# Kernel optimization log

Hardware: AMD Instinct MI355X
Metric: run time of the kernel (lower is better)

## Reference

```python
import jax, jax.numpy as jnp
import numpy as np

NUM_HEADS = 8
LN_EPS = 1e-5


def setup_inputs() -> dict:
    key = jax.random.key(0)
    ks = jax.random.split(key, 9)
    B, C, H, W = 8, 512, 32, 32
    s = 1.0 / np.sqrt(C)
    return {
        "f_curr": jax.random.normal(ks[0], (B, C, H, W), dtype=jnp.float32),
        "f_prev": jax.random.normal(ks[1], (B, C, H, W), dtype=jnp.float32),
        "f_next": jax.random.normal(ks[2], (B, C, H, W), dtype=jnp.float32),
        "Wq": jax.random.normal(ks[3], (C, C), dtype=jnp.float32) * s,
        "Wk": jax.random.normal(ks[4], (C, C), dtype=jnp.float32) * s,
        "Wv": jax.random.normal(ks[5], (C, C), dtype=jnp.float32) * s,
        "Wo": jax.random.normal(ks[6], (C, C), dtype=jnp.float32) * s,
        "gamma": jnp.ones((C,), dtype=jnp.float32),
        "beta": jnp.zeros((C,), dtype=jnp.float32),
    }


def _flatten(f):
    # [B,C,H,W] -> [B, H*W, C]
    B, C, H, W = f.shape
    return f.reshape(B, C, H * W).transpose(0, 2, 1)


def reference(f_curr, f_prev, f_next, Wq, Wk, Wv, Wo, gamma, beta):
    B, C, H, W = f_curr.shape
    N = H * W
    hd = C // NUM_HEADS
    scale = hd ** -0.5

    curr_flat = _flatten(f_curr)                              # [B,N,C]
    neigh_flat = jnp.concatenate([_flatten(f_prev), _flatten(f_next)], axis=1)  # [B,2N,C]

    # torch Linear (no bias): y = x @ W.T
    Q = curr_flat @ Wq.T                                      # [B,N,C]
    K = neigh_flat @ Wk.T                                     # [B,2N,C]
    V = neigh_flat @ Wv.T                                     # [B,2N,C]

    def split_heads(t, L):
        return t.reshape(B, L, NUM_HEADS, hd).transpose(0, 2, 1, 3)  # [B,h,L,hd]

    Qh = split_heads(Q, N)
    Kh = split_heads(K, 2 * N)
    Vh = split_heads(V, 2 * N)

    scores = jnp.einsum("bhnd,bhmd->bhnm", Qh, Kh) * scale    # [B,h,N,2N]
    attn = jax.nn.softmax(scores, axis=-1)
    out = jnp.einsum("bhnm,bhmd->bhnd", attn, Vh)             # [B,h,N,hd]

    out = out.transpose(0, 2, 1, 3).reshape(B, N, C)          # merge heads
    out = curr_flat + out @ Wo.T                              # residual

    # LayerNorm over channel dim
    mu = jnp.mean(out, axis=-1, keepdims=True)
    var = jnp.mean(jnp.square(out - mu), axis=-1, keepdims=True)
    out = (out - mu) * jax.lax.rsqrt(var + LN_EPS) * gamma + beta

    return out.transpose(0, 2, 1).reshape(B, C, H, W)
```

## Files before the change

### kernel.cpp

```cpp
#include <hip/hip_runtime.h>
#include <hip/hip_bf16.h>
#include <math.h>

#define NH 8
#define HD 64
#define CH 512
#define NT 1024
#define NB 8

typedef __bf16 bf16_t;
typedef bf16_t bf16x8 __attribute__((ext_vector_type(8)));
typedef bf16_t bf16x4 __attribute__((ext_vector_type(4)));
typedef float  f32x4  __attribute__((ext_vector_type(4)));
typedef float  f32x16 __attribute__((ext_vector_type(16)));
typedef unsigned u32x4 __attribute__((ext_vector_type(4)));

#define MFMA16(a, b, c) __builtin_amdgcn_mfma_f32_16x16x32_bf16((a), (b), (c), 0, 0, 0)
#define MFMA32(a, b, c) __builtin_amdgcn_mfma_f32_32x32x16_bf16((a), (b), (c), 0, 0, 0)
#define EXP2(x) __builtin_amdgcn_exp2f(x)

__device__ __forceinline__ void gload16(const void* g, void* l) {
    __builtin_amdgcn_global_load_lds(
        (const __attribute__((address_space(1))) void*)g,
        (__attribute__((address_space(3))) void*)l, 16, 0, 0);
}

__device__ __forceinline__ unsigned cvtpk(float lo, float hi) {
    unsigned r;
    asm("v_cvt_pk_bf16_f32 %0, %1, %2" : "=v"(r) : "v"(lo), "v"(hi));
    return r;
}

__device__ __forceinline__ void plswap(unsigned& a, unsigned& b) {
    asm("v_permlane32_swap_b32 %0, %1" : "+v"(a), "+v"(b));
}

__global__ __launch_bounds__(256) void prep_kernel(
    const float* __restrict__ fc, const float* __restrict__ fp,
    const float* __restrict__ fn, bf16_t* __restrict__ Xc,
    bf16_t* __restrict__ Xn)
{
    __shared__ __align__(16) bf16_t tile[64 * 64];
    const int t = threadIdx.x;
    const int y = blockIdx.y;
    const int b = y / 3, ft = y % 3;
    const int c0 = (blockIdx.x & 7) * 64;
    const int n0 = (blockIdx.x >> 3) * 64;

    const float* src; bf16_t* dst;
    if (ft == 0)      { src = fc + (size_t)b * CH * NT; dst = Xc + (size_t)b * NT * CH; }
    else if (ft == 1) { src = fp + (size_t)b * CH * NT; dst = Xn + (size_t)b * 2 * NT * CH; }
    else              { src = fn + (size_t)b * CH * NT; dst = Xn + (size_t)b * 2 * NT * CH + (size_t)NT * CH; }

    const int nb = t & 15, cb = t >> 4;
    float4 ld[4];
#pragma unroll
    for (int i = 0; i < 4; ++i)
        ld[i] = *(const float4*)(src + (size_t)(c0 + cb * 4 + i) * NT + n0 + nb * 4);
    const float* lf = (const float*)ld;
#pragma unroll
    for (int j = 0; j < 4; ++j) {
        int n = nb * 4 + j;
        int v = (n >> 2) & 14;
        bf16x4 wv = { (bf16_t)lf[0 * 4 + j], (bf16_t)lf[1 * 4 + j],
                      (bf16_t)lf[2 * 4 + j], (bf16_t)lf[3 * 4 + j] };
        *(bf16x4*)(tile + n * 64 + ((cb ^ v) * 4)) = wv;
    }
    __syncthreads();
#pragma unroll
    for (int i = 0; i < 2; ++i) {
        int gid = t + i * 256;
        int n = gid >> 3, c16 = gid & 7;
        int v = (n >> 2) & 14;
        bf16x8 val = *(const bf16x8*)(tile + n * 64 + (((2 * c16) ^ v) * 4));
        *(bf16x8*)(dst + (size_t)(n0 + n) * CH + c0 + c16 * 8) = val;
    }
}

__global__ __launch_bounds__(256) void wcvt_kernel(
    const float* __restrict__ Wq, const float* __restrict__ Wk,
    const float* __restrict__ Wv, const float* __restrict__ Wo,
    bf16_t* __restrict__ Wb, float* __restrict__ SQz)
{
    const int m = blockIdx.y;
    const float* src = (m == 0) ? Wq : (m == 1) ? Wk : (m == 2) ? Wv : Wo;
    bf16_t* dst = Wb + (size_t)m * CH * CH;
    int gid = blockIdx.x * 256 + threadIdx.x;
    float4 v = *(const float4*)(src + (size_t)gid * 4);
    bf16x4 o = { (bf16_t)v.x, (bf16_t)v.y, (bf16_t)v.z, (bf16_t)v.w };
    *(bf16x4*)(dst + (size_t)gid * 4) = o;
    if (m == 0 && blockIdx.x < 16) {
        f32x4 zz = {0.f, 0.f, 0.f, 0.f};
        *(f32x4*)(SQz + (size_t)(blockIdx.x * 256 + threadIdx.x) * 4) = zz;
    }
}

template <bool SWAP>
__device__ __forceinline__ void gemm_core(const bf16_t* __restrict__ A,
                                          const bf16_t* __restrict__ B,
                                          bf16_t* aT0, bf16_t* bT0,
                                          bf16_t* aT1, bf16_t* bT1,
                                          f32x4 acc[4][4])
{
    const int t = threadIdx.x, w = t >> 6, lane = t & 63;
    const int lid = lane & 15, quad = lane >> 4;
    const int wm = w >> 1, wn = w & 1;
    const int l4 = lane >> 2, k4 = lane & 3;

#define GSTAGE(k0, aT, bT)                                                     \
    {                                                                          \
        _Pragma("unroll")                                                      \
        for (int i = 0; i < 2; ++i) {                                          \
            int q = w * 2 + i;                                 \
            int row = q * 16 + l4;                                             \
            int kk = k4 ^ ((row >> 1) & 3);                                    \
            gload16(A + (size_t)row * CH + (k0) + kk * 8, (aT) + q * 512);     \
            gload16(B + (size_t)row * CH + (k0) + kk * 8, (bT) + q * 512);     \
        }                                                                      \
    }

    GSTAGE(0, aT0, bT0);
    __syncthreads();

    for (int kt = 0; kt < 16; ++kt) {
        const int cur = kt & 1;
        const bf16_t* aTr = cur ? aT1 : aT0;
        const bf16_t* bTr = cur ? bT1 : bT0;
        if (kt < 15) {
            bf16_t* aTw = cur ? aT0 : aT1;
            bf16_t* bTw = cur ? bT0 : bT1;
            GSTAGE((kt + 1) * 32, aTw, bTw);
        }

        const bf16_t* mT = SWAP ? bTr : aTr;
        const bf16_t* nT = SWAP ? aTr : bTr;
        bf16x8 mf[4], nf[4];
#pragma unroll
        for (int i = 0; i < 4; ++i) {
            int row = wm * 64 + i * 16 + lid;
            int kw = quad ^ ((row >> 1) & 3);
            mf[i] = *(const bf16x8*)(mT + row * 32 + kw * 8);
        }
#pragma unroll
        for (int i = 0; i < 4; ++i) {
            int row = wn * 64 + i * 16 + lid;
            int kw = quad ^ ((row >> 1) & 3);
            nf[i] = *(const bf16x8*)(nT + row * 32 + kw * 8);
        }
        __builtin_amdgcn_s_setprio(1);
#pragma unroll
        for (int mi = 0; mi < 4; ++mi)
#pragma unroll
            for (int ni = 0; ni < 4; ++ni)
                acc[mi][ni] = MFMA16(mf[mi], nf[ni], acc[mi][ni]);
        __builtin_amdgcn_s_setprio(0);
        __syncthreads();
    }
#undef GSTAGE
}

__global__ __launch_bounds__(256) void qkv_kernel(
    const bf16_t* __restrict__ Xc, const bf16_t* __restrict__ Xn,
    const bf16_t* __restrict__ Wb,
    bf16_t* __restrict__ Qn, bf16_t* __restrict__ Kn, bf16_t* __restrict__ Vt)
{
    __shared__ __align__(16) bf16_t aT0[128 * 32];
    __shared__ __align__(16) bf16_t bT0[128 * 32];
    __shared__ __align__(16) bf16_t aT1[128 * 32];
    __shared__ __align__(16) bf16_t bT1[128 * 32];
    const int bx = blockIdx.x, b = blockIdx.y;
    const int t = threadIdx.x, w = t >> 6, lane = t & 63;
    const int lid = lane & 15, quad = lane >> 4;
    const int wm = w >> 1, wn = w & 1;
    const float QSC = 0.125f * 1.44269504f;

    f32x4 acc[4][4] = {};

    if (bx < 96) {
        const bf16_t* A; const bf16_t* B; bf16_t* O; float scale;
        if (bx < 32) {
            int nt = bx >> 2, ct = bx & 3;
            A = Xc + (size_t)b * NT * CH + (size_t)nt * 128 * CH;
            B = Wb + (size_t)0 * CH * CH + (size_t)ct * 128 * CH;
            O = Qn + (size_t)b * NT * CH + (size_t)nt * 128 * CH + ct * 128;
            scale = QSC;
        } else {
            int j = bx - 32, nt = j >> 2, ct = j & 3;
            A = Xn + (size_t)b * 2 * NT * CH + (size_t)nt * 128 * CH;
            B = Wb + (size_t)1 * CH * CH + (size_t)ct * 128 * CH;
            O = Kn + (size_t)b * 2 * NT * CH + (size_t)nt * 128 * CH + ct * 128;
            scale = 1.0f;
        }
        gemm_core<false>(A, B, aT0, bT0, aT1, bT1, acc);
#pragma unroll
        for (int mi = 0; mi < 4; ++mi)
#pragma unroll
            for (int ni = 0; ni < 4; ++ni)
#pragma unroll
                for (int r = 0; r < 4; ++r) {
                    int n  = wm * 64 + mi * 16 + quad * 4 + r;
                    int co = wn * 64 + ni * 16 + lid;
                    O[(size_t)n * CH + co] = (bf16_t)(acc[mi][ni][r] * scale);
                }
    } else {
        int j = bx - 96, nt = j >> 2, ct = j & 3;
        const bf16_t* A = Xn + (size_t)b * 2 * NT * CH + (size_t)nt * 128 * CH;
        const bf16_t* B = Wb + (size_t)2 * CH * CH + (size_t)ct * 128 * CH;
        bf16_t* O = Vt + (size_t)b * CH * 2 * NT + (size_t)ct * 128 * 2 * NT + nt * 128;
        gemm_core<true>(A, B, aT0, bT0, aT1, bT1, acc);
#pragma unroll
        for (int mi = 0; mi < 4; ++mi)
#pragma unroll
            for (int ni = 0; ni < 4; ++ni)
#pragma unroll
                for (int r = 0; r < 4; ++r) {
                    int co_l  = wm * 64 + mi * 16 + quad * 4 + r;
                    int key_l = wn * 64 + ni * 16 + lid;
                    O[(size_t)co_l * (2 * NT) + key_l] = (bf16_t)acc[mi][ni][r];
                }
    }
}

__global__ __launch_bounds__(256, 2) void attn_kernel(
    const bf16_t* __restrict__ Qn, const bf16_t* __restrict__ Kn,
    const bf16_t* __restrict__ Vt, bf16_t* __restrict__ AOn)
{
    __shared__ __align__(16) char smem[65536];
    bf16_t* const kbuf0 = (bf16_t*)smem;
    bf16_t* const kbuf1 = (bf16_t*)(smem + 16384);
    bf16_t* const vbuf0 = (bf16_t*)(smem + 32768);
    bf16_t* const vbuf1 = (bf16_t*)(smem + 49152);
    float*  const scr_all = (float*)smem;
    bf16_t* const obuf    = (bf16_t*)(smem + 36864);
    float*  const l_scr   = (float*)(smem + 55296);

    const int t = threadIdx.x;
    const int w = t >> 6, lane = t & 63;
    const int wq = w >> 1, wk = w & 1;
    const int l31 = lane & 31, h = lane >> 5;

    const int bid = blockIdx.x;
    const int xcd = bid & 7, ii = bid >> 3;
    const int grp = xcd * 8 + (ii >> 3);
    const int qt  = ii & 7;
    const int b = grp >> 3, hh = grp & 7;
    const int q0 = qt * 128;

    const bf16_t* Qb  = Qn + ((size_t)b * NT + q0) * CH + hh * HD;
    const bf16_t* Kb  = Kn + (size_t)b * 2 * NT * CH + hh * HD;
    const bf16_t* Vtb = Vt + ((size_t)b * CH + hh * HD) * (2 * NT);
    bf16_t* AOb = AOn + ((size_t)b * NT + q0) * CH + hh * HD;

#define STAGE_KV(kbn, kw, vw)                                                  \
    {                                                                          \
        _Pragma("unroll")                                                      \
        for (int i = 0; i < 4; ++i) {                                          \
            int ck = w * 64 + i * 256 + lane;                                  \
            int kr = ck >> 3, kg = ck & 7;                                     \
            gload16(Kb + (size_t)((kbn) + kr) * CH + ((kg ^ (kr & 7)) * 8),    \
                    (kw) + (w * 64 + i * 256) * 8);                            \
            int cv = ck;                                                       \
            int vr = cv >> 4, vg = cv & 15;                                    \
            gload16(Vtb + (size_t)vr * (2 * NT) + (kbn) + ((vg ^ (vr & 15)) * 8), \
                    (vw) + (w * 64 + i * 256) * 8);                            \
        }                                                                      \
    }

    const bf16_t* Qrow = Qb + (size_t)(wq * 64 + l31) * CH + h * 8;
    bf16x8 qf[2][4];
#pragma unroll
    for (int nf = 0; nf < 2; ++nf)
#pragma unroll
        for (int ks = 0; ks < 4; ++ks)
            qf[nf][ks] = *(const bf16x8*)(Qrow + (size_t)nf * 32 * CH + ks * 16);

    STAGE_KV(0, kbuf0, vbuf0);
    __syncthreads();

    f32x16 o[2][2] = {};
    float lpart[2] = {0.f, 0.f};

    const int swk = l31 & 7;
    const int swv = l31 & 15;

    for (int kt = 0; kt < 16; ++kt) {
        const int cur = kt & 1;
        const bf16_t* const kr_buf = cur ? kbuf1 : kbuf0;
        const bf16_t* const vr_buf = cur ? vbuf1 : vbuf0;
        bf16_t* const kw_buf = cur ? kbuf0 : kbuf1;
        bf16_t* const vw_buf = cur ? vbuf0 : vbuf1;

        if (kt < 15)
            STAGE_KV((kt + 1) * 128, kw_buf, vw_buf);

#pragma unroll
        for (int mf = 0; mf < 2; ++mf) {
            const int krow = wk * 64 + mf * 32 + l31;
            bf16x8 kfm[4];
#pragma unroll
            for (int ks = 0; ks < 4; ++ks)
                kfm[ks] = *(const bf16x8*)(kr_buf + krow * 64 + (((ks * 2 + h) ^ swk) * 8));

            f32x16 s[2] = {};
            __builtin_amdgcn_s_setprio(1);
#pragma unroll
            for (int ks = 0; ks < 4; ++ks)
#pragma unroll
                for (int nf = 0; nf < 2; ++nf)
                    s[nf] = MFMA32(kfm[ks], qf[nf][ks], s[nf]);
            __builtin_amdgcn_s_setprio(0);

            bf16x8 pfrag[2][2];
#pragma unroll
            for (int nf = 0; nf < 2; ++nf) {
                float p[16];
#pragma unroll
                for (int r = 0; r < 16; ++r) p[r] = EXP2(s[nf][r]);
                lpart[nf] += ((p[0] + p[1]) + (p[2] + p[3]))
                           + ((p[4] + p[5]) + (p[6] + p[7]))
                           + ((p[8] + p[9]) + (p[10] + p[11]))
                           + ((p[12] + p[13]) + (p[14] + p[15]));
                unsigned a0 = cvtpk(p[0], p[1]),   b0 = cvtpk(p[4], p[5]);
                unsigned a1 = cvtpk(p[2], p[3]),   b1 = cvtpk(p[6], p[7]);
                unsigned a2 = cvtpk(p[8], p[9]),   b2 = cvtpk(p[12], p[13]);
                unsigned a3 = cvtpk(p[10], p[11]), b3 = cvtpk(p[14], p[15]);
                plswap(a0, b0); plswap(a1, b1); plswap(a2, b2); plswap(a3, b3);
                u32x4 f0 = { a0, a1, b0, b1 };
                u32x4 f1 = { a2, a3, b2, b3 };
                pfrag[nf][0] = __builtin_bit_cast(bf16x8, f0);
                pfrag[nf][1] = __builtin_bit_cast(bf16x8, f1);
            }

            __builtin_amdgcn_s_setprio(1);
#pragma unroll
            for (int fi = 0; fi < 2; ++fi) {
                const int ks = mf * 2 + fi;
                bf16x8 av[2];
#pragma unroll
                for (int df = 0; df < 2; ++df) {
                    int vrow = df * 32 + l31;
                    av[df] = *(const bf16x8*)(vr_buf + vrow * 128 +
                             (((wk * 8 + ks * 2 + h) ^ swv) * 8));
                }
#pragma unroll
                for (int df = 0; df < 2; ++df)
#pragma unroll
                    for (int nf = 0; nf < 2; ++nf)
                        o[df][nf] = MFMA32(av[df], pfrag[nf][fi], o[df][nf]);
            }
            __builtin_amdgcn_s_setprio(0);
        }
        __syncthreads();
    }
#undef STAGE_KV

    float l2[2];
#pragma unroll
    for (int nf = 0; nf < 2; ++nf)
        l2[nf] = lpart[nf] + __shfl_xor(lpart[nf], 32);

    if (wk == 1) {
        float* scr = scr_all + wq * 4352;
#pragma unroll
        for (int df = 0; df < 2; ++df)
#pragma unroll
            for (int nf = 0; nf < 2; ++nf) {
                int qrow = nf * 32 + l31;
#pragma unroll
                for (int g = 0; g < 4; ++g) {
                    int d = df * 32 + 8 * g + 4 * h;
                    f32x4 v = { o[df][nf][4 * g + 0], o[df][nf][4 * g + 1],
                                o[df][nf][4 * g + 2], o[df][nf][4 * g + 3] };
                    *(f32x4*)(scr + qrow * 68 + d) = v;
                }
            }
        if (h == 0) {
            l_scr[wq * 64 + 0 * 32 + l31] = l2[0];
            l_scr[wq * 64 + 1 * 32 + l31] = l2[1];
        }
    }
    __syncthreads();

    if (wk == 0) {
        const float* scr = scr_all + wq * 4352;
        float inv[2];
#pragma unroll
        for (int nf = 0; nf < 2; ++nf)
            inv[nf] = 1.0f / (l2[nf] + l_scr[wq * 64 + nf * 32 + l31]);
#pragma unroll
        for (int df = 0; df < 2; ++df)
#pragma unroll
            for (int nf = 0; nf < 2; ++nf) {
                int qrow = nf * 32 + l31;
#pragma unroll
                for (int g = 0; g < 4; ++g) {
                    int d = df * 32 + 8 * g + 4 * h;
                    f32x4 part = *(const f32x4*)(scr + qrow * 68 + d);
                    bf16x4 ov = {
                        (bf16_t)((o[df][nf][4 * g + 0] + part.x) * inv[nf]),
                        (bf16_t)((o[df][nf][4 * g + 1] + part.y) * inv[nf]),
                        (bf16_t)((o[df][nf][4 * g + 2] + part.z) * inv[nf]),
                        (bf16_t)((o[df][nf][4 * g + 3] + part.w) * inv[nf]) };
                    int qg = wq * 64 + qrow;
                    *(bf16x4*)(obuf + qg * 72 + (d ^ (qg & 24))) = ov;
                }
            }
    }
    __syncthreads();

#pragma unroll
    for (int i = 0; i < 4; ++i) {
        int gid = t + i * 256;
        int qr = gid >> 3, c8 = (gid & 7) * 8;
        *(bf16x8*)(AOb + (size_t)qr * CH + c8) =
            *(const bf16x8*)(obuf + qr * 72 + (c8 ^ (qr & 24)));
    }
}

__global__ __launch_bounds__(256) void proj_kernel(
    const bf16_t* __restrict__ AOn, const bf16_t* __restrict__ Wb,
    const float* __restrict__ fc, float* __restrict__ Zt,
    float* __restrict__ Ssum, float* __restrict__ Ssq)
{
    __shared__ __align__(16) bf16_t aT0[128 * 32];
    __shared__ __align__(16) bf16_t bT0[128 * 32];
    __shared__ __align__(16) bf16_t aT1[128 * 32];
    __shared__ __align__(16) bf16_t bT1[128 * 32];
    const int bx = blockIdx.x, b = blockIdx.y;
    const int nt = bx >> 2, ct = bx & 3;
    const int t = threadIdx.x, w = t >> 6, lane = t & 63;
    const int lid = lane & 15, quad = lane >> 4;
    const int wm = w >> 1, wn = w & 1;

    const bf16_t* A = AOn + (size_t)b * NT * CH + (size_t)nt * 128 * CH;
    const bf16_t* B = Wb + (size_t)3 * CH * CH + (size_t)ct * 128 * CH;

    f32x4 acc[4][4] = {};
    gemm_core<true>(A, B, aT0, bT0, aT1, bT1, acc);

    const size_t bofs = (size_t)b * CH * NT;
    float sP[4] = {0.f, 0.f, 0.f, 0.f}, qP[4] = {0.f, 0.f, 0.f, 0.f};
#pragma unroll
    for (int mi = 0; mi < 4; ++mi)
#pragma unroll
        for (int ni = 0; ni < 4; ++ni)
#pragma unroll
            for (int r = 0; r < 4; ++r) {
                int co_l = wm * 64 + mi * 16 + quad * 4 + r;
                int n_l  = wn * 64 + ni * 16 + lid;
                size_t idx = bofs + (size_t)(ct * 128 + co_l) * NT + nt * 128 + n_l;
                float z = acc[mi][ni][r] + fc[idx];
                Zt[idx] = z;
                sP[ni] += z;
                qP[ni] += z * z;
            }
#pragma unroll
    for (int ni = 0; ni < 4; ++ni) {
        sP[ni] += __shfl_xor(sP[ni], 16);  sP[ni] += __shfl_xor(sP[ni], 32);
        qP[ni] += __shfl_xor(qP[ni], 16);  qP[ni] += __shfl_xor(qP[ni], 32);
    }
    __syncthreads();
    float* sRed = (float*)aT0;
    float* qRed = sRed + 256;
    if (quad == 0) {
#pragma unroll
        for (int ni = 0; ni < 4; ++ni) {
            sRed[w * 64 + ni * 16 + lid] = sP[ni];
            qRed[w * 64 + ni * 16 + lid] = qP[ni];
        }
    }
    __syncthreads();
    if (t < 128) {
        float s = sRed[t] + sRed[128 + t];
        float q = qRed[t] + qRed[128 + t];
        atomicAdd(&Ssum[(size_t)b * NT + nt * 128 + t], s);
        atomicAdd(&Ssq [(size_t)b * NT + nt * 128 + t], q);
    }
}

__global__ __launch_bounds__(256) void apply_kernel(
    const float* __restrict__ Zt, const float* __restrict__ Ssum,
    const float* __restrict__ Ssq, const float* __restrict__ gamma,
    const float* __restrict__ beta, float* __restrict__ out)
{
    const int row = blockIdx.x;
    const int co = row & 511, b = row >> 9;
    const int t = threadIdx.x;
    const float g = gamma[co], be = beta[co];
    const size_t base = (size_t)row * NT + t * 4;
    f32x4 z  = *(const f32x4*)(Zt + base);
    f32x4 S  = *(const f32x4*)(Ssum + (size_t)b * NT + t * 4);
    f32x4 Q2 = *(const f32x4*)(Ssq  + (size_t)b * NT + t * 4);
    f32x4 o;
#pragma unroll
    for (int c = 0; c < 4; ++c) {
        float mu  = S[c] * (1.0f / 512.0f);
        float var = Q2[c] * (1.0f / 512.0f) - mu * mu;
        float rs  = rsqrtf(var + 1e-5f);
        o[c] = (z[c] - mu) * rs * g + be;
    }
    *(f32x4*)(out + base) = o;
}

extern "C" void kernel_launch(void* const* d_in, const int* in_sizes, int n_in,
                              void* d_out, int out_size, void* d_ws, size_t ws_size,
                              hipStream_t stream)
{
    (void)in_sizes; (void)n_in; (void)out_size; (void)ws_size;
    const float* fc    = (const float*)d_in[0];
    const float* fp    = (const float*)d_in[1];
    const float* fn    = (const float*)d_in[2];
    const float* Wq    = (const float*)d_in[3];
    const float* Wk    = (const float*)d_in[4];
    const float* Wv    = (const float*)d_in[5];
    const float* Wo    = (const float*)d_in[6];
    const float* gamma = (const float*)d_in[7];
    const float* beta  = (const float*)d_in[8];
    float* out = (float*)d_out;

    char* ws = (char*)d_ws;
    bf16_t* Xn  = (bf16_t*)(ws);
    bf16_t* Qn  = (bf16_t*)(ws + 16777216);
    bf16_t* Kn  = (bf16_t*)(ws + 25165824);
    bf16_t* Xc  = (bf16_t*)(ws + 41943040);
    bf16_t* AOn = Xc;
    bf16_t* Vt  = (bf16_t*)(ws + 50331648);
    bf16_t* Wb  = (bf16_t*)(ws + 67108864);
    float*  Ssum = (float*)(ws + 69206016);
    float*  Ssq  = (float*)(ws + 69238784);
    float*  Zt  = (float*)(ws);

    prep_kernel<<<dim3(128, 24), 256, 0, stream>>>(fc, fp, fn, Xc, Xn);
    wcvt_kernel<<<dim3(256, 4), 256, 0, stream>>>(Wq, Wk, Wv, Wo, Wb, Ssum);
    qkv_kernel<<<dim3(160, 8), 256, 0, stream>>>(Xc, Xn, Wb, Qn, Kn, Vt);
    attn_kernel<<<dim3(512), 256, 0, stream>>>(Qn, Kn, Vt, AOn);
    proj_kernel<<<dim3(32, 8), 256, 0, stream>>>(AOn, Wb, fc, Zt, Ssum, Ssq);
    apply_kernel<<<4096, 256, 0, stream>>>(Zt, Ssum, Ssq, gamma, beta, out);
}
```

Before: 207.5 us.

## Halve attention tile sizes to double block count and occupancy

The attention kernel moves from 128-query by 128-key tiles to 64-query by 64-key tiles, halving shared memory to 32KB and raising launch bounds to 4 blocks per CU, with 1024 blocks instead of 512. The aim is more resident waves and better latency hiding on the many-CU GPU. In exchange, each K/V tile is reused by half as many queries, so K/V traffic from L2 doubles, there are twice as many loop iterations and barriers, and the V swizzle layout is changed to match.

```diff
diff --git a/kernel.cpp b/kernel.cpp
--- a/kernel.cpp
+++ b/kernel.cpp
@@ -221,18 +221,18 @@
     }
 }
 
-__global__ __launch_bounds__(256, 2) void attn_kernel(
+__global__ __launch_bounds__(256, 4) void attn_kernel(
     const bf16_t* __restrict__ Qn, const bf16_t* __restrict__ Kn,
     const bf16_t* __restrict__ Vt, bf16_t* __restrict__ AOn)
 {
-    __shared__ __align__(16) char smem[65536];
+    __shared__ __align__(16) char smem[32768];
     bf16_t* const kbuf0 = (bf16_t*)smem;
-    bf16_t* const kbuf1 = (bf16_t*)(smem + 16384);
-    bf16_t* const vbuf0 = (bf16_t*)(smem + 32768);
-    bf16_t* const vbuf1 = (bf16_t*)(smem + 49152);
+    bf16_t* const kbuf1 = (bf16_t*)(smem + 8192);
+    bf16_t* const vbuf0 = (bf16_t*)(smem + 16384);
+    bf16_t* const vbuf1 = (bf16_t*)(smem + 24576);
     float*  const scr_all = (float*)smem;
-    bf16_t* const obuf    = (bf16_t*)(smem + 36864);
-    float*  const l_scr   = (float*)(smem + 55296);
+    bf16_t* const obuf    = (bf16_t*)(smem + 17920);
+    float*  const l_scr   = (float*)(smem + 27136);
 
     const int t = threadIdx.x;
     const int w = t >> 6, lane = t & 63;
@@ -241,10 +241,10 @@
 
     const int bid = blockIdx.x;
     const int xcd = bid & 7, ii = bid >> 3;
-    const int grp = xcd * 8 + (ii >> 3);
-    const int qt  = ii & 7;
+    const int grp = xcd * 8 + (ii >> 4);
+    const int qt  = ii & 15;
     const int b = grp >> 3, hh = grp & 7;
-    const int q0 = qt * 128;
+    const int q0 = qt * 64;
 
     const bf16_t* Qb  = Qn + ((size_t)b * NT + q0) * CH + hh * HD;
     const bf16_t* Kb  = Kn + (size_t)b * 2 * NT * CH + hh * HD;
@@ -254,162 +254,127 @@
 #define STAGE_KV(kbn, kw, vw)                                                  \
     {                                                                          \
         _Pragma("unroll")                                                      \
-        for (int i = 0; i < 4; ++i) {                                          \
+        for (int i = 0; i < 2; ++i) {                                          \
             int ck = w * 64 + i * 256 + lane;                                  \
             int kr = ck >> 3, kg = ck & 7;                                     \
             gload16(Kb + (size_t)((kbn) + kr) * CH + ((kg ^ (kr & 7)) * 8),    \
                     (kw) + (w * 64 + i * 256) * 8);                            \
-            int cv = ck;                                                       \
-            int vr = cv >> 4, vg = cv & 15;                                    \
-            gload16(Vtb + (size_t)vr * (2 * NT) + (kbn) + ((vg ^ (vr & 15)) * 8), \
+            gload16(Vtb + (size_t)kr * (2 * NT) + (kbn) + ((kg ^ (kr & 7)) * 8), \
                     (vw) + (w * 64 + i * 256) * 8);                            \
         }                                                                      \
     }
 
-    const bf16_t* Qrow = Qb + (size_t)(wq * 64 + l31) * CH + h * 8;
-    bf16x8 qf[2][4];
-#pragma unroll
-    for (int nf = 0; nf < 2; ++nf)
-#pragma unroll
-        for (int ks = 0; ks < 4; ++ks)
-            qf[nf][ks] = *(const bf16x8*)(Qrow + (size_t)nf * 32 * CH + ks * 16);
+    const bf16_t* Qrow = Qb + (size_t)(wq * 32 + l31) * CH + h * 8;
+    bf16x8 qf[4];
+#pragma unroll
+    for (int ks = 0; ks < 4; ++ks)
+        qf[ks] = *(const bf16x8*)(Qrow + ks * 16);
 
     STAGE_KV(0, kbuf0, vbuf0);
     __syncthreads();
 
-    f32x16 o[2][2] = {};
-    float lpart[2] = {0.f, 0.f};
-
-    const int swk = l31 & 7;
-    const int swv = l31 & 15;
-
-    for (int kt = 0; kt < 16; ++kt) {
+    f32x16 o[2] = {};
+    float lpart = 0.f;
+
+    for (int kt = 0; kt < 32; ++kt) {
         const int cur = kt & 1;
         const bf16_t* const kr_buf = cur ? kbuf1 : kbuf0;
         const bf16_t* const vr_buf = cur ? vbuf1 : vbuf0;
         bf16_t* const kw_buf = cur ? kbuf0 : kbuf1;
         bf16_t* const vw_buf = cur ? vbuf0 : vbuf1;
 
-        if (kt < 15)
-            STAGE_KV((kt + 1) * 128, kw_buf, vw_buf);
-
-#pragma unroll
-        for (int mf = 0; mf < 2; ++mf) {
-            const int krow = wk * 64 + mf * 32 + l31;
-            bf16x8 kfm[4];
-#pragma unroll
-            for (int ks = 0; ks < 4; ++ks)
-                kfm[ks] = *(const bf16x8*)(kr_buf + krow * 64 + (((ks * 2 + h) ^ swk) * 8));
-
-            f32x16 s[2] = {};
-            __builtin_amdgcn_s_setprio(1);
-#pragma unroll
-            for (int ks = 0; ks < 4; ++ks)
-#pragma unroll
-                for (int nf = 0; nf < 2; ++nf)
-                    s[nf] = MFMA32(kfm[ks], qf[nf][ks], s[nf]);
-            __builtin_amdgcn_s_setprio(0);
-
-            bf16x8 pfrag[2][2];
-#pragma unroll
-            for (int nf = 0; nf < 2; ++nf) {
-                float p[16];
-#pragma unroll
-                for (int r = 0; r < 16; ++r) p[r] = EXP2(s[nf][r]);
-                lpart[nf] += ((p[0] + p[1]) + (p[2] + p[3]))
-                           + ((p[4] + p[5]) + (p[6] + p[7]))
-                           + ((p[8] + p[9]) + (p[10] + p[11]))
-                           + ((p[12] + p[13]) + (p[14] + p[15]));
-                unsigned a0 = cvtpk(p[0], p[1]),   b0 = cvtpk(p[4], p[5]);
-                unsigned a1 = cvtpk(p[2], p[3]),   b1 = cvtpk(p[6], p[7]);
-                unsigned a2 = cvtpk(p[8], p[9]),   b2 = cvtpk(p[12], p[13]);
-                unsigned a3 = cvtpk(p[10], p[11]), b3 = cvtpk(p[14], p[15]);
-                plswap(a0, b0); plswap(a1, b1); plswap(a2, b2); plswap(a3, b3);
-                u32x4 f0 = { a0, a1, b0, b1 };
-                u32x4 f1 = { a2, a3, b2, b3 };
-                pfrag[nf][0] = __builtin_bit_cast(bf16x8, f0);
-                pfrag[nf][1] = __builtin_bit_cast(bf16x8, f1);
+        if (kt < 31)
+            STAGE_KV((kt + 1) * 64, kw_buf, vw_buf);
+
+        const int krow = wk * 32 + l31;
+        bf16x8 kfm[4];
+#pragma unroll
+        for (int ks = 0; ks < 4; ++ks)
+            kfm[ks] = *(const bf16x8*)(kr_buf + krow * 64 + (((ks * 2 + h) ^ (krow & 7)) * 8));
+
+        f32x16 s = {};
+        __builtin_amdgcn_s_setprio(1);
+#pragma unroll
+        for (int ks = 0; ks < 4; ++ks)
+            s = MFMA32(kfm[ks], qf[ks], s);
+        __builtin_amdgcn_s_setprio(0);
+
+        float p[16];
+#pragma unroll
+        for (int r = 0; r < 16; ++r) p[r] = EXP2(s[r]);
+        lpart += ((p[0] + p[1]) + (p[2] + p[3]))
+               + ((p[4] + p[5]) + (p[6] + p[7]))
+               + ((p[8] + p[9]) + (p[10] + p[11]))
+               + ((p[12] + p[13]) + (p[14] + p[15]));
+        unsigned a0 = cvtpk(p[0], p[1]),   b0 = cvtpk(p[4], p[5]);
+        unsigned a1 = cvtpk(p[2], p[3]),   b1 = cvtpk(p[6], p[7]);
+        unsigned a2 = cvtpk(p[8], p[9]),   b2 = cvtpk(p[12], p[13]);
+        unsigned a3 = cvtpk(p[10], p[11]), b3 = cvtpk(p[14], p[15]);
+        plswap(a0, b0); plswap(a1, b1); plswap(a2, b2); plswap(a3, b3);
+        u32x4 f0 = { a0, a1, b0, b1 };
+        u32x4 f1 = { a2, a3, b2, b3 };
+        bf16x8 pfrag0 = __builtin_bit_cast(bf16x8, f0);
+        bf16x8 pfrag1 = __builtin_bit_cast(bf16x8, f1);
+
+        __builtin_amdgcn_s_setprio(1);
+#pragma unroll
+        for (int fi = 0; fi < 2; ++fi) {
+            const bf16x8 pf = fi ? pfrag1 : pfrag0;
+            bf16x8 av[2];
+#pragma unroll
+            for (int df = 0; df < 2; ++df) {
+                int vrow = df * 32 + l31;
+                int g = wk * 4 + fi * 2 + h;
+                av[df] = *(const bf16x8*)(vr_buf + vrow * 64 + ((g ^ (vrow & 7)) * 8));
             }
-
-            __builtin_amdgcn_s_setprio(1);
-#pragma unroll
-            for (int fi = 0; fi < 2; ++fi) {
-                const int ks = mf * 2 + fi;
-                bf16x8 av[2];
-#pragma unroll
-                for (int df = 0; df < 2; ++df) {
-                    int vrow = df * 32 + l31;
-                    av[df] = *(const bf16x8*)(vr_buf + vrow * 128 +
-                             (((wk * 8 + ks * 2 + h) ^ swv) * 8));
-                }
-#pragma unroll
-                for (int df = 0; df < 2; ++df)
-#pragma unroll
-                    for (int nf = 0; nf < 2; ++nf)
-                        o[df][nf] = MFMA32(av[df], pfrag[nf][fi], o[df][nf]);
+#pragma unroll
+            for (int df = 0; df < 2; ++df)
+                o[df] = MFMA32(av[df], pf, o[df]);
+        }
+        __builtin_amdgcn_s_setprio(0);
+        __syncthreads();
+    }
+#undef STAGE_KV
+
+    float l2 = lpart + __shfl_xor(lpart, 32);
+
+    if (wk == 1) {
+        float* scr = scr_all + wq * 2176;
+#pragma unroll
+        for (int df = 0; df < 2; ++df)
+#pragma unroll
+            for (int g = 0; g < 4; ++g) {
+                int d = df * 32 + 8 * g + 4 * h;
+                f32x4 v = { o[df][4 * g + 0], o[df][4 * g + 1],
+                            o[df][4 * g + 2], o[df][4 * g + 3] };
+                *(f32x4*)(scr + l31 * 68 + d) = v;
             }
-            __builtin_amdgcn_s_setprio(0);
-        }
-        __syncthreads();
-    }
-#undef STAGE_KV
-
-    float l2[2];
-#pragma unroll
-    for (int nf = 0; nf < 2; ++nf)
-        l2[nf] = lpart[nf] + __shfl_xor(lpart[nf], 32);
-
-    if (wk == 1) {
-        float* scr = scr_all + wq * 4352;
+        if (h == 0) l_scr[wq * 32 + l31] = l2;
+    }
+    __syncthreads();
+
+    if (wk == 0) {
+        const float* scr = scr_all + wq * 2176;
+        float inv = 1.0f / (l2 + l_scr[wq * 32 + l31]);
 #pragma unroll
         for (int df = 0; df < 2; ++df)
 #pragma unroll
-            for (int nf = 0; nf < 2; ++nf) {
-                int qrow = nf * 32 + l31;
-#pragma unroll
-                for (int g = 0; g < 4; ++g) {
-                    int d = df * 32 + 8 * g + 4 * h;
-                    f32x4 v = { o[df][nf][4 * g + 0], o[df][nf][4 * g + 1],
-                                o[df][nf][4 * g + 2], o[df][nf][4 * g + 3] };
-                    *(f32x4*)(scr + qrow * 68 + d) = v;
-                }
+            for (int g = 0; g < 4; ++g) {
+                int d = df * 32 + 8 * g + 4 * h;
+                f32x4 part = *(const f32x4*)(scr + l31 * 68 + d);
+                bf16x4 ov = {
+                    (bf16_t)((o[df][4 * g + 0] + part.x) * inv),
+                    (bf16_t)((o[df][4 * g + 1] + part.y) * inv),
+                    (bf16_t)((o[df][4 * g + 2] + part.z) * inv),
+                    (bf16_t)((o[df][4 * g + 3] + part.w) * inv) };
+                int qg = wq * 32 + l31;
+                *(bf16x4*)(obuf + qg * 72 + (d ^ (qg & 24))) = ov;
             }
-        if (h == 0) {
-            l_scr[wq * 64 + 0 * 32 + l31] = l2[0];
-            l_scr[wq * 64 + 1 * 32 + l31] = l2[1];
-        }
-    }
-    __syncthreads();
-
-    if (wk == 0) {
-        const float* scr = scr_all + wq * 4352;
-        float inv[2];
-#pragma unroll
-        for (int nf = 0; nf < 2; ++nf)
-            inv[nf] = 1.0f / (l2[nf] + l_scr[wq * 64 + nf * 32 + l31]);
-#pragma unroll
-        for (int df = 0; df < 2; ++df)
-#pragma unroll
-            for (int nf = 0; nf < 2; ++nf) {
-                int qrow = nf * 32 + l31;
-#pragma unroll
-                for (int g = 0; g < 4; ++g) {
-                    int d = df * 32 + 8 * g + 4 * h;
-                    f32x4 part = *(const f32x4*)(scr + qrow * 68 + d);
-                    bf16x4 ov = {
-                        (bf16_t)((o[df][nf][4 * g + 0] + part.x) * inv[nf]),
-                        (bf16_t)((o[df][nf][4 * g + 1] + part.y) * inv[nf]),
-                        (bf16_t)((o[df][nf][4 * g + 2] + part.z) * inv[nf]),
-                        (bf16_t)((o[df][nf][4 * g + 3] + part.w) * inv[nf]) };
-                    int qg = wq * 64 + qrow;
-                    *(bf16x4*)(obuf + qg * 72 + (d ^ (qg & 24))) = ov;
-                }
-            }
-    }
-    __syncthreads();
-
-#pragma unroll
-    for (int i = 0; i < 4; ++i) {
+    }
+    __syncthreads();
+
+#pragma unroll
+    for (int i = 0; i < 2; ++i) {
         int gid = t + i * 256;
         int qr = gid >> 3, c8 = (gid & 7) * 8;
         *(bf16x8*)(AOb + (size_t)qr * CH + c8) =
@@ -533,7 +498,7 @@
     prep_kernel<<<dim3(128, 24), 256, 0, stream>>>(fc, fp, fn, Xc, Xn);
     wcvt_kernel<<<dim3(256, 4), 256, 0, stream>>>(Wq, Wk, Wv, Wo, Wb, Ssum);
     qkv_kernel<<<dim3(160, 8), 256, 0, stream>>>(Xc, Xn, Wb, Qn, Kn, Vt);
-    attn_kernel<<<dim3(512), 256, 0, stream>>>(Qn, Kn, Vt, AOn);
+    attn_kernel<<<dim3(1024), 256, 0, stream>>>(Qn, Kn, Vt, AOn);
     proj_kernel<<<dim3(32, 8), 256, 0, stream>>>(AOn, Wb, fc, Zt, Ssum, Ssq);
     apply_kernel<<<4096, 256, 0, stream>>>(Zt, Ssum, Ssq, gamma, beta, out);
 }
```

Result: no change. 210.7 us (+1.6%).
